# Performance work log

Hardware: AMD Instinct MI355X
Metric: run time of the kernel (lower is better)

Reference implementation:

```python
import jax, jax.numpy as jnp
import numpy as np

DECAY = 0.99
EPSILON = 1e-05
N_TOKENS = 32768
EMBED_DIM = 256
NUM_EMB = 4096


def setup_inputs() -> dict:
    key = jax.random.key(0)
    k1, k2, k3 = jax.random.split(key, 3)
    return {
        "inputs": jax.random.normal(k1, (N_TOKENS, EMBED_DIM), dtype=jnp.float32),
        "codebook": jax.random.normal(k2, (NUM_EMB, EMBED_DIM), dtype=jnp.float32),
        "ema_w": jax.random.normal(k3, (NUM_EMB, EMBED_DIM), dtype=jnp.float32),
        "ema_cluster_size": jnp.zeros((NUM_EMB,), dtype=jnp.float32),
    }


def reference(inputs, codebook, ema_w, ema_cluster_size):
    K, D = codebook.shape
    flat = inputs.reshape(-1, D)  # [N, D]
    distances = (
        jnp.sum(flat * flat, axis=1, keepdims=True)
        + jnp.sum(codebook * codebook, axis=1)
        - 2.0 * flat @ codebook.T
    )
    encoding_indices = jnp.argmin(distances, axis=1)  # [N]
    encodings = jax.nn.one_hot(encoding_indices, K, dtype=flat.dtype)  # [N, K]
    quantized = codebook[encoding_indices].reshape(inputs.shape)  # [N, D]

    # EMA update (training branch). dw = encodings.T @ flat expressed as a
    # segment sum to avoid a second [N,K]-sized contraction pass.
    dw = jax.ops.segment_sum(flat, encoding_indices, num_segments=K)  # [K, D]
    counts = jax.ops.segment_sum(
        jnp.ones((flat.shape[0],), dtype=flat.dtype), encoding_indices, num_segments=K
    )  # [K]
    new_ema_w = ema_w * DECAY + (1.0 - DECAY) * dw
    cs = ema_cluster_size * DECAY + (1.0 - DECAY) * counts
    n = jnp.sum(cs)
    cs = (cs + EPSILON) / (n + K * EPSILON) * n  # laplace smoothing
    new_codebook = new_ema_w / cs[:, None]
    return quantized, encodings, new_codebook, new_ema_w, cs
```

## Files before the change

kernel.cpp:

```cpp
#include <hip/hip_runtime.h>
#include <hip/hip_bf16.h>

#define NTOK 32768
#define KEMB 4096
#define DDIM 256
#define DECAYF 0.99f
#define EPSF 1e-5f
#define KSPLIT 256
#define FLAG_THETA 0.11f
#define PRUNE_MARGIN 0.28f
#define SBIAS 4096.0f

#define B_AHAT  0ull
#define B_BHAT  16777216ull
#define B_PART  18874368ull
#define B_CE    52428800ull
#define B_CNTI  52445184ull
#define B_CSP   52461568ull
#define B_OFFS  52477952ull
#define B_NPTR  52494336ull
#define B_TIDX  52494400ull
#define B_TLIST 52887616ull
#define B_DW    53018688ull

#define OFF_Q  0ull
#define OFF_E  8388608ull
#define OFF_CB 142606336ull
#define OFF_W  143654912ull
#define OFF_CS 144703488ull

typedef __attribute__((ext_vector_type(8))) _Float16 f16x8;
typedef __attribute__((ext_vector_type(4))) _Float16 f16x4;
typedef __attribute__((ext_vector_type(4))) float f32x4;

__global__ __launch_bounds__(256) void prep_kernel(const float* __restrict__ xg,
                                                   const float* __restrict__ cbg,
                                                   _Float16* __restrict__ Ahat,
                                                   _Float16* __restrict__ Bhat,
                                                   float* __restrict__ ce,
                                                   int* __restrict__ countsI,
                                                   float4* __restrict__ dwv) {
    int b = blockIdx.x;
    int tid = threadIdx.x;
    if (b < 4096) {
        size_t gid = (size_t)b * 256 + tid;
        const float* sp = xg + gid * 8;
        f16x8 v;
        #pragma unroll
        for (int t = 0; t < 8; ++t) v[t] = (_Float16)sp[t];
        *(f16x8*)(Ahat + gid * 8) = v;
    } else if (b < 5120) {
        int k = (b - 4096) * 4 + (tid >> 6);
        int lane = tid & 63;
        float4 v = *(const float4*)(cbg + (size_t)k * DDIM + lane * 4);
        f16x4 h;
        h[0] = (_Float16)v.x; h[1] = (_Float16)v.y;
        h[2] = (_Float16)v.z; h[3] = (_Float16)v.w;
        *(f16x4*)(Bhat + (size_t)k * DDIM + lane * 4) = h;
        float s = v.x * v.x + v.y * v.y + v.z * v.z + v.w * v.w;
        #pragma unroll
        for (int o = 32; o > 0; o >>= 1) s += __shfl_down(s, o);
        if (lane == 0) ce[k] = s;
    } else if (b < 5136) {
        countsI[(b - 5120) * 256 + tid] = 0;
    } else {
        float4 z = {0.f, 0.f, 0.f, 0.f};
        dwv[(size_t)(b - 5136) * 256 + tid] = z;
    }
}

__global__ __launch_bounds__(256) void gemm_argmin_kernel(
        const _Float16* __restrict__ Ahat,
        const _Float16* __restrict__ Bhat,
        const float* __restrict__ ceg,
        float2* __restrict__ part,
        float* __restrict__ enc) {
    __shared__ _Float16 As[128 * 64];
    __shared__ _Float16 Bs[128 * 64];
    const int tid  = threadIdx.x;
    const int lane = tid & 63;
    const int wave = tid >> 6;
    const int wm = wave >> 1, wn = wave & 1;

    int lin = blockIdx.y * 32 + blockIdx.x;
    lin = (lin & 7) * 1024 + (lin >> 3);
    const int nb = lin & 31, mb = lin >> 5;

    const int col = lane & 15, q = lane >> 4;
    const int cswz = q ^ (col & 7);

    const int srow = tid >> 3;
    const int sswz = (tid & 7) ^ (srow & 7);
    const _Float16* ag = Ahat + (size_t)(mb * 128 + srow) * KSPLIT + sswz * 8;
    const _Float16* bg = Bhat + (size_t)(nb * 128 + srow) * KSPLIT + sswz * 8;

    f32x4 zero = {0.f, 0.f, 0.f, 0.f};
    f32x4 acc[4][4];
    #pragma unroll
    for (int i = 0; i < 4; ++i)
        #pragma unroll
        for (int j = 0; j < 4; ++j) acc[i][j] = zero;

    for (int kt = 0; kt < KSPLIT / 64; ++kt) {
        __syncthreads();
        #pragma unroll
        for (int n = 0; n < 4; ++n) {
            __builtin_amdgcn_global_load_lds(
                (const __attribute__((address_space(1))) void*)(ag + (size_t)n * 32 * KSPLIT + kt * 64),
                (__attribute__((address_space(3))) void*)(As + n * 2048 + tid * 8), 16, 0, 0);
            __builtin_amdgcn_global_load_lds(
                (const __attribute__((address_space(1))) void*)(bg + (size_t)n * 32 * KSPLIT + kt * 64),
                (__attribute__((address_space(3))) void*)(Bs + n * 2048 + tid * 8), 16, 0, 0);
        }
        __syncthreads();

        const f16x8* Av = (const f16x8*)As;
        const f16x8* Bv = (const f16x8*)Bs;
        #pragma unroll
        for (int ks = 0; ks < 2; ++ks) {
            f16x8 a[4], b[4];
            #pragma unroll
            for (int i = 0; i < 4; ++i)
                a[i] = Av[(wm * 64 + i * 16 + col) * 8 + (cswz ^ (ks * 4))];
            #pragma unroll
            for (int j = 0; j < 4; ++j)
                b[j] = Bv[(wn * 64 + j * 16 + col) * 8 + (cswz ^ (ks * 4))];
            #pragma unroll
            for (int i = 0; i < 4; ++i)
                #pragma unroll
                for (int j = 0; j < 4; ++j)
                    acc[i][j] = __builtin_amdgcn_mfma_f32_16x16x32_f16(a[i], b[j], acc[i][j], 0, 0, 0);
        }
    }

    float ce_j[4];
    #pragma unroll
    for (int j = 0; j < 4; ++j) ce_j[j] = ceg[nb * 128 + wn * 64 + j * 16 + col];

    #pragma unroll
    for (int i = 0; i < 4; ++i) {
        #pragma unroll
        for (int r = 0; r < 4; ++r) {
            float p1 = 3.4e38f, p2 = 3.4e38f;
            #pragma unroll
            for (int j = 0; j < 4; ++j) {
                float s = ce_j[j] - 2.0f * acc[i][j][r] + SBIAS;
                int loc = j * 16 + col;
                float sp = __int_as_float((__float_as_int(s) & ~63) | loc);
                if (sp < p1) { p2 = p1; p1 = sp; }
                else if (sp < p2) { p2 = sp; }
            }
            #pragma unroll
            for (int m = 1; m < 16; m <<= 1) {
                float o1 = __shfl_xor(p1, m, 16);
                float o2 = __shfl_xor(p2, m, 16);
                float lo = fminf(p1, o1);
                float hi = fmaxf(p1, o1);
                p2 = fminf(hi, fminf(p2, o2));
                p1 = lo;
            }
            if (col == i * 4 + r) {
                int mrow = mb * 128 + wm * 64 + i * 16 + q * 4 + r;
                float2 p;
                p.x = p1; p.y = p2;
                part[(size_t)mrow * 64 + nb * 2 + wn] = p;
            }
        }
    }

    {
        f32x4* ez = (f32x4*)(enc + (size_t)lin * 16384) + tid;
        f32x4 z4 = {0.f, 0.f, 0.f, 0.f};
        #pragma unroll
        for (int v = 0; v < 16; ++v)
            __builtin_nontemporal_store(z4, ez + v * 256);
    }
}

__global__ __launch_bounds__(256) void post_kernel(const float* __restrict__ xg,
                                                   const float* __restrict__ cb,
                                                   const float2* __restrict__ part,
                                                   int* __restrict__ tokIdx,
                                                   int* __restrict__ countsI,
                                                   float* __restrict__ quant,
                                                   float* __restrict__ enc) {
    int row = blockIdx.x * 4 + (threadIdx.x >> 6);
    int lane = threadIdx.x & 63;
    float2 p = part[(size_t)row * 64 + lane];
    float own = p.x;
    float b1 = p.x, b2 = p.y;
    #pragma unroll
    for (int m = 1; m < 64; m <<= 1) {
        float o1 = __shfl_xor(b1, m);
        float o2 = __shfl_xor(b2, m);
        float lo = fminf(b1, o1);
        float hi = fmaxf(b1, o1);
        b2 = fminf(hi, fminf(b2, o2));
        b1 = lo;
    }
    int kfin;
    {
        unsigned long long wmask = __ballot(own == b1);
        int wl = __ffsll(wmask) - 1;
        kfin = wl * 64 + (__float_as_int(b1) & 63);
    }
    if (b2 - b1 < FLAG_THETA) {
        unsigned long long mask = __ballot(own <= b1 + PRUNE_MARGIN);
        double best = 1e300;
        int bi = 0x7fffffff;
        const float* xr = xg + (size_t)row * DDIM;
        while (mask) {
            int c = __ffsll(mask) - 1;
            mask &= mask - 1;
            int k = c * 64 + lane;
            const float* e = cb + (size_t)k * DDIM;
            double s = 0.0;
            for (int d4 = 0; d4 < DDIM / 4; ++d4) {
                float4 e4 = *(const float4*)(e + d4 * 4);
                float4 x4 = *(const float4*)(xr + d4 * 4);
                double e0 = (double)e4.x, e1 = (double)e4.y;
                double e2 = (double)e4.z, e3 = (double)e4.w;
                s += e0 * (e0 - 2.0 * (double)x4.x) + e1 * (e1 - 2.0 * (double)x4.y)
                   + e2 * (e2 - 2.0 * (double)x4.z) + e3 * (e3 - 2.0 * (double)x4.w);
            }
            if (s < best || (s == best && k < bi)) { best = s; bi = k; }
        }
        #pragma unroll
        for (int m = 1; m < 64; m <<= 1) {
            double ob = __shfl_xor(best, m);
            int   oi  = __shfl_xor(bi, m);
            if (ob < best || (ob == best && oi < bi)) { best = ob; bi = oi; }
        }
        kfin = bi;
    }
    if (lane == 0) {
        tokIdx[row] = kfin;
        atomicAdd(countsI + kfin, 1);
        enc[(size_t)row * KEMB + kfin] = 1.0f;
    }
    float4 e = *(const float4*)(cb + (size_t)kfin * DDIM + lane * 4);
    *(float4*)(quant + (size_t)row * DDIM + lane * 4) = e;
}

__global__ __launch_bounds__(256) void scan_cs_kernel(const int* __restrict__ countsI,
                                                      const float* __restrict__ ema_cs,
                                                      int* __restrict__ offs,
                                                      float* __restrict__ cs_pre,
                                                      float* __restrict__ nptr) {
    __shared__ int part[256];
    __shared__ float npart[256];
    __shared__ int pref[257];
    int tid = threadIdx.x;
    int local[16];
    int s = 0;
    float ns = 0.0f;
    #pragma unroll
    for (int i = 0; i < 16; ++i) {
        int c = countsI[tid * 16 + i];
        local[i] = c;
        s += c;
        float csp = ema_cs[tid * 16 + i] * DECAYF + (1.0f - DECAYF) * (float)c;
        cs_pre[tid * 16 + i] = csp;
        ns += csp;
    }
    part[tid] = s;
    npart[tid] = ns;
    __syncthreads();
    if (tid == 0) {
        pref[0] = 0;
        float nn = 0.0f;
        for (int i = 0; i < 256; ++i) {
            pref[i + 1] = pref[i] + part[i];
            nn += npart[i];
        }
        nptr[0] = nn;
    }
    __syncthreads();
    int run = pref[tid];
    #pragma unroll
    for (int i = 0; i < 16; ++i) { offs[tid * 16 + i] = run; run += local[i]; }
}

__global__ __launch_bounds__(256) void filllist_kernel(const int* __restrict__ tokIdx,
                                                       int* __restrict__ offs,
                                                       int* __restrict__ tlist) {
    int t = blockIdx.x * 256 + threadIdx.x;
    int k = tokIdx[t];
    int slot = atomicAdd(offs + k, 1);
    tlist[slot] = t;
}

#define SEG_CHUNK 32
__global__ __launch_bounds__(256) void segdw_kernel(const float* __restrict__ xg,
                                                    const int* __restrict__ tlist,
                                                    const int* __restrict__ tokIdx,
                                                    float* __restrict__ dw) {
    int tid = threadIdx.x;
    int s0 = blockIdx.x * SEG_CHUNK;
    float acc = 0.0f;
    int curk = -1;
    for (int s = s0; s < s0 + SEG_CHUNK; ++s) {
        int t = tlist[s];
        int k = tokIdx[t];
        if (k != curk) {
            if (curk >= 0) atomicAdd(dw + (size_t)curk * DDIM + tid, acc);
            acc = 0.0f;
            curk = k;
        }
        acc += xg[(size_t)t * DDIM + tid];
    }
    if (curk >= 0) atomicAdd(dw + (size_t)curk * DDIM + tid, acc);
}

__global__ __launch_bounds__(256) void epi_kernel(const float* __restrict__ ema_w,
                                                  const float* __restrict__ dw,
                                                  const float* __restrict__ cs_pre,
                                                  const float* __restrict__ nptr,
                                                  float* __restrict__ new_cb,
                                                  float* __restrict__ new_w,
                                                  float* __restrict__ cs_out) {
    int gid = blockIdx.x * 256 + threadIdx.x;
    int k = gid >> 8, d = gid & 255;
    float n = *nptr;
    float csp = cs_pre[k];
    float cs = (csp + EPSF) / (n + (float)KEMB * EPSF) * n;
    float w = ema_w[gid] * DECAYF + (1.0f - DECAYF) * dw[gid];
    new_w[gid] = w;
    new_cb[gid] = w / cs;
    if (d == 0) cs_out[k] = cs;
}

extern "C" void kernel_launch(void* const* d_in, const int* in_sizes, int n_in,
                              void* d_out, int out_size, void* d_ws, size_t ws_size,
                              hipStream_t stream) {
    const float* xg     = (const float*)d_in[0];
    const float* cbg    = (const float*)d_in[1];
    const float* ema_w  = (const float*)d_in[2];
    const float* ema_cs = (const float*)d_in[3];

    float* out = (float*)d_out;
    unsigned char* wsb = (unsigned char*)d_ws;

    float* quant  = out + OFF_Q;
    float* enc    = out + OFF_E;
    float* new_cb = out + OFF_CB;
    float* new_w  = out + OFF_W;
    float* cs_out = out + OFF_CS;

    _Float16* Ahat = (_Float16*)(wsb + B_AHAT);
    _Float16* Bhat = (_Float16*)(wsb + B_BHAT);
    float2* part   = (float2*)(wsb + B_PART);
    float* ce      = (float*)(wsb + B_CE);
    int*   countsI = (int*)(wsb + B_CNTI);
    float* cs_pre  = (float*)(wsb + B_CSP);
    int*   offs    = (int*)(wsb + B_OFFS);
    float* nptr    = (float*)(wsb + B_NPTR);
    int*   tokIdx  = (int*)(wsb + B_TIDX);
    int*   tlist   = (int*)(wsb + B_TLIST);
    float* dw      = (float*)(wsb + B_DW);

    prep_kernel<<<6160, 256, 0, stream>>>(xg, cbg, Ahat, Bhat, ce, countsI, (float4*)dw);
    gemm_argmin_kernel<<<dim3(KEMB / 128, NTOK / 128), 256, 0, stream>>>(Ahat, Bhat, ce, part, enc);
    post_kernel<<<NTOK / 4, 256, 0, stream>>>(xg, cbg, part, tokIdx, countsI, quant, enc);
    scan_cs_kernel<<<1, 256, 0, stream>>>(countsI, ema_cs, offs, cs_pre, nptr);
    filllist_kernel<<<NTOK / 256, 256, 0, stream>>>(tokIdx, offs, tlist);
    segdw_kernel<<<NTOK / SEG_CHUNK, 256, 0, stream>>>(xg, tlist, tokIdx, dw);
    epi_kernel<<<(KEMB * DDIM) / 256, 256, 0, stream>>>(ema_w, dw, cs_pre, nptr,
                                                        new_cb, new_w, cs_out);
}
```

Before: 735.1 us.

## Fuse segment-sum dw accumulation into post kernel via direct float atomics

The counting-sort path (prefix scan of counts, token list fill, segmented accumulation) is replaced by direct per-token atomicAdd of the input row into dw inside the post kernel that picks the argmin. This removes two kernel launches, the offset scan and the token index/list buffers, and a second read of the inputs. The cost is 32768×256 scattered float atomics, which can contend when many tokens map to the same code. Summation order also becomes nondeterministic.

```diff
diff --git a/kernel.cpp b/kernel.cpp
--- a/kernel.cpp
+++ b/kernel.cpp
@@ -17,10 +17,7 @@
 #define B_CE    52428800ull
 #define B_CNTI  52445184ull
 #define B_CSP   52461568ull
-#define B_OFFS  52477952ull
 #define B_NPTR  52494336ull
-#define B_TIDX  52494400ull
-#define B_TLIST 52887616ull
 #define B_DW    53018688ull
 
 #define OFF_Q  0ull
@@ -180,10 +177,10 @@
 __global__ __launch_bounds__(256) void post_kernel(const float* __restrict__ xg,
                                                    const float* __restrict__ cb,
                                                    const float2* __restrict__ part,
-                                                   int* __restrict__ tokIdx,
                                                    int* __restrict__ countsI,
                                                    float* __restrict__ quant,
-                                                   float* __restrict__ enc) {
+                                                   float* __restrict__ enc,
+                                                   float* __restrict__ dw) {
     int row = blockIdx.x * 4 + (threadIdx.x >> 6);
     int lane = threadIdx.x & 63;
     float2 p = part[(size_t)row * 64 + lane];
@@ -234,82 +231,42 @@
         kfin = bi;
     }
     if (lane == 0) {
-        tokIdx[row] = kfin;
         atomicAdd(countsI + kfin, 1);
         enc[(size_t)row * KEMB + kfin] = 1.0f;
     }
     float4 e = *(const float4*)(cb + (size_t)kfin * DDIM + lane * 4);
     *(float4*)(quant + (size_t)row * DDIM + lane * 4) = e;
+    {
+        float4 x4 = *(const float4*)(xg + (size_t)row * DDIM + lane * 4);
+        float* dp = dw + (size_t)kfin * DDIM + lane * 4;
+        atomicAdd(dp + 0, x4.x);
+        atomicAdd(dp + 1, x4.y);
+        atomicAdd(dp + 2, x4.z);
+        atomicAdd(dp + 3, x4.w);
+    }
 }
 
 __global__ __launch_bounds__(256) void scan_cs_kernel(const int* __restrict__ countsI,
                                                       const float* __restrict__ ema_cs,
-                                                      int* __restrict__ offs,
                                                       float* __restrict__ cs_pre,
                                                       float* __restrict__ nptr) {
-    __shared__ int part[256];
     __shared__ float npart[256];
-    __shared__ int pref[257];
     int tid = threadIdx.x;
-    int local[16];
-    int s = 0;
     float ns = 0.0f;
     #pragma unroll
     for (int i = 0; i < 16; ++i) {
         int c = countsI[tid * 16 + i];
-        local[i] = c;
-        s += c;
         float csp = ema_cs[tid * 16 + i] * DECAYF + (1.0f - DECAYF) * (float)c;
         cs_pre[tid * 16 + i] = csp;
         ns += csp;
     }
-    part[tid] = s;
     npart[tid] = ns;
     __syncthreads();
     if (tid == 0) {
-        pref[0] = 0;
         float nn = 0.0f;
-        for (int i = 0; i < 256; ++i) {
-            pref[i + 1] = pref[i] + part[i];
-            nn += npart[i];
-        }
+        for (int i = 0; i < 256; ++i) nn += npart[i];
         nptr[0] = nn;
     }
-    __syncthreads();
-    int run = pref[tid];
-    #pragma unroll
-    for (int i = 0; i < 16; ++i) { offs[tid * 16 + i] = run; run += local[i]; }
-}
-
-__global__ __launch_bounds__(256) void filllist_kernel(const int* __restrict__ tokIdx,
-                                                       int* __restrict__ offs,
-                                                       int* __restrict__ tlist) {
-    int t = blockIdx.x * 256 + threadIdx.x;
-    int k = tokIdx[t];
-    int slot = atomicAdd(offs + k, 1);
-    tlist[slot] = t;
-}
-
-#define SEG_CHUNK 32
-__global__ __launch_bounds__(256) void segdw_kernel(const float* __restrict__ xg,
-                                                    const int* __restrict__ tlist,
-                                                    const int* __restrict__ tokIdx,
-                                                    float* __restrict__ dw) {
-    int tid = threadIdx.x;
-    int s0 = blockIdx.x * SEG_CHUNK;
-    float acc = 0.0f;
-    int curk = -1;
-    for (int s = s0; s < s0 + SEG_CHUNK; ++s) {
-        int t = tlist[s];
-        int k = tokIdx[t];
-        if (k != curk) {
-            if (curk >= 0) atomicAdd(dw + (size_t)curk * DDIM + tid, acc);
-            acc = 0.0f;
-            curk = k;
-        }
-        acc += xg[(size_t)t * DDIM + tid];
-    }
-    if (curk >= 0) atomicAdd(dw + (size_t)curk * DDIM + tid, acc);
 }
 
 __global__ __launch_bounds__(256) void epi_kernel(const float* __restrict__ ema_w,
@@ -353,18 +310,13 @@
     float* ce      = (float*)(wsb + B_CE);
     int*   countsI = (int*)(wsb + B_CNTI);
     float* cs_pre  = (float*)(wsb + B_CSP);
-    int*   offs    = (int*)(wsb + B_OFFS);
     float* nptr    = (float*)(wsb + B_NPTR);
-    int*   tokIdx  = (int*)(wsb + B_TIDX);
-    int*   tlist   = (int*)(wsb + B_TLIST);
     float* dw      = (float*)(wsb + B_DW);
 
     prep_kernel<<<6160, 256, 0, stream>>>(xg, cbg, Ahat, Bhat, ce, countsI, (float4*)dw);
     gemm_argmin_kernel<<<dim3(KEMB / 128, NTOK / 128), 256, 0, stream>>>(Ahat, Bhat, ce, part, enc);
-    post_kernel<<<NTOK / 4, 256, 0, stream>>>(xg, cbg, part, tokIdx, countsI, quant, enc);
-    scan_cs_kernel<<<1, 256, 0, stream>>>(countsI, ema_cs, offs, cs_pre, nptr);
-    filllist_kernel<<<NTOK / 256, 256, 0, stream>>>(tokIdx, offs, tlist);
-    segdw_kernel<<<NTOK / SEG_CHUNK, 256, 0, stream>>>(xg, tlist, tokIdx, dw);
+    post_kernel<<<NTOK / 4, 256, 0, stream>>>(xg, cbg, part, countsI, quant, enc, dw);
+    scan_cs_kernel<<<1, 256, 0, stream>>>(countsI, ema_cs, cs_pre, nptr);
     epi_kernel<<<(KEMB * DDIM) / 256, 256, 0, stream>>>(ema_w, dw, cs_pre, nptr,
                                                         new_cb, new_w, cs_out);
 }
```

Result: slower. 853.5 us (+16.1%).
